# Performance work log

Measured on AMD Instinct MI355X. Metric: run time of the kernel, lower is better.

Reference implementation:

```python
import jax, jax.numpy as jnp
import numpy as np

B, L, E, H, K = 128, 512, 512, 256, 64


def setup_inputs() -> dict:
    key = jax.random.key(0)
    ks = jax.random.split(key, 13)
    s = 1.0 / np.sqrt(H)

    def u(k, shape):
        return jax.random.uniform(k, shape, jnp.float32, -s, s)

    return {
        "input_batch": jax.random.normal(ks[0], (B, L, E), jnp.float32),
        "labels": jax.random.randint(ks[1], (B, L), 0, K),
        "w_ih_f": u(ks[2], (4 * H, E)),
        "w_hh_f": u(ks[3], (4 * H, H)),
        "b_ih_f": u(ks[4], (4 * H,)),
        "b_hh_f": u(ks[5], (4 * H,)),
        "w_ih_b": u(ks[6], (4 * H, E)),
        "w_hh_b": u(ks[7], (4 * H, H)),
        "b_ih_b": u(ks[8], (4 * H,)),
        "b_hh_b": u(ks[9], (4 * H,)),
        "w_emit": u(ks[10], (K, 2 * H)),
        "b_emit": jnp.zeros((K,), jnp.float32),
        "transition": jax.random.normal(ks[11], (K, K), jnp.float32),
    }


def _lstm_dir(x, w_ih, w_hh, b_ih, b_hh):
    """One LSTM direction. x: (L,B,E) -> hidden states (L,B,H). PyTorch gate order i,f,g,o."""
    Hh = w_hh.shape[1]
    # input contribution for all timesteps at once: (L,B,4H)
    pre = jnp.einsum('lbe,ge->lbg', x, w_ih) + b_ih + b_hh

    def step(carry, p_t):
        h, c = carry
        g = p_t + h @ w_hh.T  # (B,4H)
        i, f, gg, o = jnp.split(g, 4, axis=-1)
        c = jax.nn.sigmoid(f) * c + jax.nn.sigmoid(i) * jnp.tanh(gg)
        h = jax.nn.sigmoid(o) * jnp.tanh(c)
        return (h, c), h

    init = (jnp.zeros((x.shape[1], Hh), x.dtype), jnp.zeros((x.shape[1], Hh), x.dtype))
    _, hs = jax.lax.scan(step, init, pre)
    return hs


def _bilstm_crf_loss(input_batch, labels, w_ih_f, w_hh_f, b_ih_f, b_hh_f,
                     w_ih_b, w_hh_b, b_ih_b, b_hh_b, w_emit, b_emit, transition):
    x = jnp.transpose(input_batch, (1, 0, 2))  # (L,B,E)
    h_f = _lstm_dir(x, w_ih_f, w_hh_f, b_ih_f, b_hh_f)
    h_b = _lstm_dir(x[::-1], w_ih_b, w_hh_b, b_ih_b, b_hh_b)[::-1]
    h = jnp.concatenate([h_f, h_b], axis=-1)  # (L,B,2H)
    emit = jnp.einsum('lbh,kh->b018'.replace('018', 'lk'), h, w_emit) + b_emit  # placeholder fixed below
    emit = jnp.einsum('lbh,kh->lbk', h, w_emit) + b_emit  # (L,B,K)
    emit = jnp.transpose(emit, (1, 0, 2))  # (B,L,K)

    # gold path score
    gold_emit = jnp.take_along_axis(emit, labels[:, :, None], axis=2)[:, :, 0]  # (B,L)
    gold_trans = transition[labels[:, :-1], labels[:, 1:]]  # (B,L-1)
    total_score = gold_emit.sum(axis=1) + gold_trans.sum(axis=1)  # (B,)

    # CRF forward algorithm (log partition), scan over timesteps 1..L-1
    def crf_step(d, e_t):
        # d: (B,K) log alpha; e_t: (B,K) emit at step t
        d = jax.nn.logsumexp(d[:, :, None] + transition[None, :, :] + e_t[:, None, :], axis=1)
        return d, None

    d0 = emit[:, 0]  # (B,K)
    dT, _ = jax.lax.scan(crf_step, d0, jnp.transpose(emit[:, 1:], (1, 0, 2)))
    log_z = jax.nn.logsumexp(dT, axis=1)  # (B,)
    return -(total_score - log_z)  # (B,)


def reference(input_batch, labels, w_ih_f, w_hh_f, b_ih_f, b_hh_f,
              w_ih_b, w_hh_b, b_ih_b, b_hh_b, w_emit, b_emit, transition):
    return _bilstm_crf_loss(input_batch, labels, w_ih_f, w_hh_f, b_ih_f, b_hh_f,
                            w_ih_b, w_hh_b, b_ih_b, b_hh_b, w_emit, b_emit, transition)
```

## Files before the change

kernel.cpp:

```cpp
#include <hip/hip_runtime.h>
#include <hip/hip_bf16.h>

#define B_   128
#define L_   512
#define E_   512
#define H_   256
#define K_   64
#define G4H  1024
#define LOG2E 1.4426950408889634f

typedef __bf16 bf16x8 __attribute__((ext_vector_type(8)));
typedef float  f32x4  __attribute__((ext_vector_type(4)));
typedef int    i32x8  __attribute__((ext_vector_type(8)));

__device__ inline unsigned short f2bf(float f) {
    unsigned int x = __builtin_bit_cast(unsigned int, f);
    unsigned int r = (x + 0x7fffu + ((x >> 16) & 1u)) >> 16;
    return (unsigned short)r;
}
__device__ inline float bf2f(unsigned short u) {
    unsigned int x = ((unsigned int)u) << 16;
    return __builtin_bit_cast(float, x);
}
__device__ inline unsigned int pack2(float lo, float hi) {
    return (unsigned int)f2bf(lo) | ((unsigned int)f2bf(hi) << 16);
}
__device__ inline float ex2(float x) { return __builtin_amdgcn_exp2f(x); }
__device__ inline float rcp_(float x) { return __builtin_amdgcn_rcpf(x); }

__device__ inline void gl_lds16(const unsigned short* g, unsigned short* l) {
    __builtin_amdgcn_global_load_lds(
        (const __attribute__((address_space(1))) unsigned int*)g,
        (__attribute__((address_space(3))) unsigned int*)l, 16, 0, 0);
}

__global__ void setup_convert(const float* __restrict__ whh_f, const float* __restrict__ whh_b,
                              const float* __restrict__ wemit,
                              const float* __restrict__ wihf, const float* __restrict__ wihb,
                              const float* __restrict__ bihf, const float* __restrict__ bhhf,
                              const float* __restrict__ bihb, const float* __restrict__ bhhb,
                              unsigned char* __restrict__ whh8,
                              unsigned short* __restrict__ wemit_bf,
                              unsigned short* __restrict__ wp,
                              float* __restrict__ bias_p) {
    int i = blockIdx.x * 256 + threadIdx.x;
    if (i < 262144) {
        int j = 2 * i;
        float v0 = (j < 262144) ? whh_f[j] : whh_b[j - 262144];
        float v1 = (j + 1 < 262144) ? whh_f[j + 1] : whh_b[j + 1 - 262144];
        int pk = __builtin_amdgcn_cvt_pk_fp8_f32(v0 * LOG2E, v1 * LOG2E, 0, false);
        ((unsigned short*)whh8)[i] = (unsigned short)(pk & 0xffff);
    }
    if (i < K_ * 2 * H_) wemit_bf[i] = f2bf(wemit[i]);
    if (i < 131072) {
        int rp = i >> 6;
        int k8 = (i & 63) * 8;
        int dd = rp >> 10, np = rp & 1023;
        int srow = (np & 3) * 256 + (np >> 2);
        const float* src = (dd == 0 ? wihf : wihb) + (size_t)srow * 512 + k8;
        float4 a  = *reinterpret_cast<const float4*>(src);
        float4 b2 = *reinterpret_cast<const float4*>(src + 4);
        uint4 pk = { pack2(a.x * LOG2E, a.y * LOG2E), pack2(a.z * LOG2E, a.w * LOG2E),
                     pack2(b2.x * LOG2E, b2.y * LOG2E), pack2(b2.z * LOG2E, b2.w * LOG2E) };
        *reinterpret_cast<uint4*>(wp + (size_t)rp * 512 + k8) = pk;
    }
    if (i < 2048) {
        int dd = i >> 10, np = i & 1023;
        int srow = (np & 3) * 256 + (np >> 2);
        bias_p[i] = ((dd == 0) ? (bihf[srow] + bhhf[srow]) : (bihb[srow] + bhhb[srow])) * LOG2E;
    }
}

__global__ void convert_x(const float* __restrict__ x, unsigned short* __restrict__ xb) {
    int i = blockIdx.x * 256 + threadIdx.x;
    float4 a = reinterpret_cast<const float4*>(x)[i * 2];
    float4 b = reinterpret_cast<const float4*>(x)[i * 2 + 1];
    uint4 p = { pack2(a.x, a.y), pack2(a.z, a.w), pack2(b.x, b.y), pack2(b.z, b.w) };
    reinterpret_cast<uint4*>(xb)[i] = p;
}

__global__ __launch_bounds__(256) void pre_gemm(
    const unsigned short* __restrict__ xb,
    const unsigned short* __restrict__ wp,
    const float* __restrict__ bias_p,
    unsigned short* __restrict__ pre3)
{
    __shared__ unsigned short A_lds[128 * 32];
    __shared__ unsigned short B_lds[128 * 32];

    int nt = blockIdx.x, mt = blockIdx.y;
    int tid = threadIdx.x;
    int n0 = nt * 128;
    int b  = mt >> 2, l0 = (mt & 3) * 128;
    int w = tid >> 6, lane = tid & 63;
    int q = lane >> 4, ln = lane & 15;
    int wm = (w >> 1) * 64, wn = (w & 1) * 64;

    f32x4 acc[4][4];
    #pragma unroll
    for (int i = 0; i < 4; ++i)
        #pragma unroll
        for (int j = 0; j < 4; ++j) acc[i][j] = (f32x4){0.f, 0.f, 0.f, 0.f};

    int r_ = tid >> 2, kp = (tid & 3) * 8;
    const unsigned short* asrc0 = xb + ((size_t)b * 512 + l0 + r_) * 512 + kp;
    const unsigned short* asrc1 = asrc0 + (size_t)64 * 512;
    const unsigned short* bsrc0 = wp + (size_t)(n0 + r_) * 512 + kp;
    const unsigned short* bsrc1 = bsrc0 + (size_t)64 * 512;
    unsigned short* adst0 = &A_lds[tid * 8];
    unsigned short* adst1 = &A_lds[2048 + tid * 8];
    unsigned short* bdst0 = &B_lds[tid * 8];
    unsigned short* bdst1 = &B_lds[2048 + tid * 8];

    for (int kc = 0; kc < 16; ++kc) {
        int k0 = kc * 32;
        gl_lds16(asrc0 + k0, adst0);
        gl_lds16(asrc1 + k0, adst1);
        gl_lds16(bsrc0 + k0, bdst0);
        gl_lds16(bsrc1 + k0, bdst1);
        __syncthreads();

        bf16x8 af[4], bfv[4];
        #pragma unroll
        for (int ms = 0; ms < 4; ++ms)
            af[ms] = *reinterpret_cast<const bf16x8*>(&A_lds[(wm + ms * 16 + ln) * 32 + q * 8]);
        #pragma unroll
        for (int ns = 0; ns < 4; ++ns)
            bfv[ns] = *reinterpret_cast<const bf16x8*>(&B_lds[(wn + ns * 16 + ln) * 32 + q * 8]);
        #pragma unroll
        for (int ms = 0; ms < 4; ++ms)
            #pragma unroll
            for (int ns = 0; ns < 4; ++ns)
                acc[ms][ns] = __builtin_amdgcn_mfma_f32_16x16x32_bf16(af[ms], bfv[ns], acc[ms][ns], 0, 0, 0);
        __syncthreads();
    }

    #pragma unroll
    for (int ns = 0; ns < 4; ++ns) {
        int n = n0 + wn + ns * 16 + ln;
        float bias = bias_p[n];
        int dsel = n >> 10, np = n & 1023;
        #pragma unroll
        for (int ms = 0; ms < 4; ++ms) {
            #pragma unroll
            for (int rg = 0; rg < 4; ++rg) {
                int l = l0 + wm + ms * 16 + q * 4 + rg;
                pre3[(((size_t)dsel * 128 + b) * 512 + l) * 1024 + np] = f2bf(acc[ms][ns][rg] + bias);
            }
        }
    }
}

__global__ __launch_bounds__(512, 2) void lstm_scan(
    const unsigned short* __restrict__ pre3,
    const unsigned char* __restrict__ whh8,
    unsigned short* __restrict__ hcat)
{
    __shared__ unsigned char h_lds[2][16 * 272];

    int wg = blockIdx.x;
    int d = wg >> 7, b = wg & 127;
    int tid = threadIdx.x, w = tid >> 6, lane = tid & 63;
    int q = lane >> 4, ln = lane & 15;

    const unsigned char* whh_d = whh8 + (size_t)d * (1024 * 256);
    const unsigned short* pre_wg = pre3 + ((size_t)d * 128 + b) * (512 * 1024);

    i32x8 wh[4][2][2];
    #pragma unroll
    for (int g = 0; g < 4; ++g)
        #pragma unroll
        for (int s = 0; s < 2; ++s) {
            int row = g * 256 + (w + 8 * s) * 16 + ln;
            #pragma unroll
            for (int kc = 0; kc < 2; ++kc)
                wh[g][s][kc] = *reinterpret_cast<const i32x8*>(
                    whh_d + (size_t)row * 256 + kc * 128 + q * 32);
        }

    for (int i = tid; i < (2 * 16 * 272) / 4; i += 512) ((int*)h_lds)[i] = 0;

    bool act = (lane < 32);
    int s_  = (lane >> 4) & 1;
    int col = (w + 8 * s_) * 16 + ln;

    ushort4 p0 = {0,0,0,0}, p1 = {0,0,0,0};
    if (act) {
        int la  = (d == 0) ? 0 : (L_ - 1);
        int lb_ = (d == 0) ? 1 : (L_ - 2);
        p0 = *reinterpret_cast<const ushort4*>(pre_wg + (size_t)la * 1024 + col * 4);
        p1 = *reinterpret_cast<const ushort4*>(pre_wg + (size_t)lb_ * 1024 + col * 4);
    }
    __syncthreads();

    float cst = 0.f;

    for (int t = 0; t < L_; ++t) {
        int p = t & 1;
        int l = (d == 0) ? t : (L_ - 1 - t);

        ushort4 p2 = {0,0,0,0};
        if (act) {
            int t2 = (t + 2 < L_) ? (t + 2) : (L_ - 1);
            int l2 = (d == 0) ? t2 : (L_ - 1 - t2);
            p2 = *reinterpret_cast<const ushort4*>(pre_wg + (size_t)l2 * 1024 + col * 4);
        }

        f32x4 acc[4][2];
        #pragma unroll
        for (int g = 0; g < 4; ++g) {
            acc[g][0] = (f32x4){0.f, 0.f, 0.f, 0.f};
            acc[g][1] = (f32x4){0.f, 0.f, 0.f, 0.f};
        }
        #pragma unroll
        for (int kc = 0; kc < 2; ++kc) {
            const unsigned char* ab = &h_lds[p][ln * 272 + kc * 128 + q * 32];
            uint4 a0 = *reinterpret_cast<const uint4*>(ab);
            uint4 a1 = *reinterpret_cast<const uint4*>(ab + 16);
            i32x8 af = { (int)a0.x, (int)a0.y, (int)a0.z, (int)a0.w,
                         (int)a1.x, (int)a1.y, (int)a1.z, (int)a1.w };
            #pragma unroll
            for (int g = 0; g < 4; ++g)
                #pragma unroll
                for (int s = 0; s < 2; ++s)
                    acc[g][s] = __builtin_amdgcn_mfma_scale_f32_16x16x128_f8f6f4(
                        af, wh[g][s][kc], acc[g][s], 0, 0,
                        0, 0x7f7f7f7f, 0, 0x7f7f7f7f);
        }

        float gv[4];
        #pragma unroll
        for (int g = 0; g < 4; ++g) {
            float lo = __shfl(acc[g][0][0], ln);
            float hi = __shfl(acc[g][1][0], ln);
            gv[g] = s_ ? hi : lo;
        }

        if (act) {
            float vi = gv[0] + bf2f(p0.x);
            float vf = gv[1] + bf2f(p0.y);
            float vg = gv[2] + bf2f(p0.z);
            float vo = gv[3] + bf2f(p0.w);
            float ei  = ex2(vi);
            float e2g = ex2(vg + vg);
            float itg = (ei * (e2g - 1.f)) * rcp_((1.f + ei) * (1.f + e2g));
            float sf  = rcp_(1.f + ex2(-vf));
            float cn  = fmaf(sf, cst, itg);
            cst = cn;
            float tc  = fmaf(-2.f, rcp_(1.f + ex2((2.f * LOG2E) * cn)), 1.f);
            float so  = rcp_(1.f + ex2(-vo));
            float hn  = so * tc;
            int pk = __builtin_amdgcn_cvt_pk_fp8_f32(hn, hn, 0, false);
            h_lds[p ^ 1][col] = (unsigned char)(pk & 0xff);
            hcat[((size_t)l * 128 + b) * 512 + d * 256 + col] = f2bf(hn);
        }
        __syncthreads();

        p0 = p1; p1 = p2;
    }
}

__global__ __launch_bounds__(256) void emit_gemm(
    const unsigned short* __restrict__ hcat,
    const unsigned short* __restrict__ wemit,
    const float* __restrict__ bemit,
    float* __restrict__ emit)
{
    int m0 = blockIdx.x * 64;
    int tid = threadIdx.x, w = tid >> 6, lane = tid & 63;
    int quad = lane >> 4, ln = lane & 15;
    int mrow = m0 + w * 16;

    f32x4 acc[4];
    #pragma unroll
    for (int i = 0; i < 4; ++i) acc[i] = (f32x4){0.f, 0.f, 0.f, 0.f};

    const unsigned short* arow = hcat + (size_t)(mrow + ln) * 512;
    #pragma unroll 4
    for (int kc = 0; kc < 16; ++kc) {
        bf16x8 af = *reinterpret_cast<const bf16x8*>(arow + kc * 32 + quad * 8);
        #pragma unroll
        for (int T = 0; T < 4; ++T) {
            bf16x8 bfv = *reinterpret_cast<const bf16x8*>(wemit + (size_t)(T * 16 + ln) * 512 + kc * 32 + quad * 8);
            acc[T] = __builtin_amdgcn_mfma_f32_16x16x32_bf16(af, bfv, acc[T], 0, 0, 0);
        }
    }
    #pragma unroll
    for (int T = 0; T < 4; ++T) {
        int k = T * 16 + ln;
        float bias = bemit[k];
        #pragma unroll
        for (int rg = 0; rg < 4; ++rg) {
            int m = mrow + quad * 4 + rg;
            int ll = m >> 7, bidx = m & 127;
            emit[((size_t)bidx * L_ + ll) * K_ + k] = acc[T][rg] + bias;
        }
    }
}

__global__ __launch_bounds__(64) void crf_kernel(
    const float* __restrict__ emit,
    const int* __restrict__ labels,
    const float* __restrict__ trans,
    float* __restrict__ out)
{
    __shared__ float els[64];
    int b = blockIdx.x, lane = threadIdx.x;
    const float* eb = emit + (size_t)b * L_ * K_;
    const int* lb = labels + (size_t)b * L_;

    float gold = 0.f;
    for (int t = lane; t < L_; t += 64) gold += eb[(size_t)t * K_ + lb[t]];
    for (int t = lane; t < L_ - 1; t += 64) gold += trans[lb[t] * K_ + lb[t + 1]];
    #pragma unroll
    for (int off = 32; off; off >>= 1) gold += __shfl_down(gold, off);

    float expT[64];
    #pragma unroll
    for (int i = 0; i < 64; ++i) expT[i] = __expf(trans[i * K_ + lane]);

    float dstate = eb[lane];
    float enext = eb[K_ + lane];
    for (int t = 1; t < L_; ++t) {
        float ecur = enext;
        if (t + 1 < L_) enext = eb[(size_t)(t + 1) * K_ + lane];
        float M = __builtin_amdgcn_readfirstlane(dstate);
        float e = __expf(dstate - M);
        __syncthreads();
        els[lane] = e;
        __syncthreads();
        float s = 0.f;
        #pragma unroll
        for (int i = 0; i < 64; i += 4) {
            float4 ev = *reinterpret_cast<const float4*>(&els[i]);
            s = fmaf(ev.x, expT[i], s);
            s = fmaf(ev.y, expT[i + 1], s);
            s = fmaf(ev.z, expT[i + 2], s);
            s = fmaf(ev.w, expT[i + 3], s);
        }
        dstate = M + __logf(s) + ecur;
    }
    float M = __builtin_amdgcn_readfirstlane(dstate);
    float e = __expf(dstate - M);
    float s = e;
    #pragma unroll
    for (int off = 32; off; off >>= 1) s += __shfl_xor(s, off);
    float logZ = M + __logf(s);
    if (lane == 0) out[b] = -(gold - logZ);
}

#define OFF_PRE    ((size_t)0)
#define OFF_EMIT   OFF_PRE
#define OFF_HCAT   ((size_t)268435456)
#define OFF_XB     OFF_HCAT
#define OFF_WHH8   ((size_t)(OFF_HCAT + 67108864))
#define OFF_WEMIT  ((size_t)(OFF_WHH8 + 524288))
#define OFF_WP     ((size_t)(OFF_WEMIT + 65536))
#define OFF_BIAS   ((size_t)(OFF_WP + 2097152))

extern "C" void kernel_launch(void* const* d_in, const int* in_sizes, int n_in,
                              void* d_out, int out_size, void* d_ws, size_t ws_size,
                              hipStream_t stream) {
    const float* x      = (const float*)d_in[0];
    const int*   labels = (const int*)d_in[1];
    const float* wihf   = (const float*)d_in[2];
    const float* whhf   = (const float*)d_in[3];
    const float* bihf   = (const float*)d_in[4];
    const float* bhhf   = (const float*)d_in[5];
    const float* wihb   = (const float*)d_in[6];
    const float* whhb   = (const float*)d_in[7];
    const float* bihb   = (const float*)d_in[8];
    const float* bhhb   = (const float*)d_in[9];
    const float* wemit  = (const float*)d_in[10];
    const float* bemit  = (const float*)d_in[11];
    const float* trans  = (const float*)d_in[12];
    float* out = (float*)d_out;

    char* ws = (char*)d_ws;
    unsigned short* pre3   = (unsigned short*)(ws + OFF_PRE);
    unsigned short* hcat   = (unsigned short*)(ws + OFF_HCAT);
    unsigned short* xb     = (unsigned short*)(ws + OFF_XB);
    float*          emit   = (float*)(ws + OFF_EMIT);
    unsigned char*  whh8   = (unsigned char*)(ws + OFF_WHH8);
    unsigned short* we_bf  = (unsigned short*)(ws + OFF_WEMIT);
    unsigned short* wp     = (unsigned short*)(ws + OFF_WP);
    float*          bias_p = (float*)(ws + OFF_BIAS);

    setup_convert<<<1024, 256, 0, stream>>>(whhf, whhb, wemit, wihf, wihb,
                                            bihf, bhhf, bihb, bhhb,
                                            whh8, we_bf, wp, bias_p);
    convert_x<<<16384, 256, 0, stream>>>(x, xb);
    pre_gemm<<<dim3(16, 512), 256, 0, stream>>>(xb, wp, bias_p, pre3);
    lstm_scan<<<256, 512, 0, stream>>>(pre3, whh8, hcat);
    emit_gemm<<<1024, 256, 0, stream>>>(hcat, we_bf, bemit, emit);
    crf_kernel<<<128, 64, 0, stream>>>(emit, labels, trans, out);
}
```

Measured before the change: 1.087 ms.

## Batch 16 sequences per LSTM workgroup via MFMA columns; double-buffer CRF LDS

The LSTM scan now uses the 16 MFMA columns for 16 batch elements in one workgroup, so 16 workgroups run instead of 256. Previously each workgroup handled a single sequence and wasted 15 of 16 MFMA columns. Each lane now computes four gate cells per slice, writes packed fp8/bf16 outputs, and prefetches pre-activations two steps ahead with an unrolled pair of steps. The CRF kernel double-buffers its LDS exchange to drop one barrier per step and splits the dot product into four accumulators. The risk is that only 16 CUs carry the serial scan, which adds more per-step latency per workgroup.

```diff
diff --git a/kernel.cpp b/kernel.cpp
--- a/kernel.cpp
+++ b/kernel.cpp
@@ -12,6 +12,7 @@
 typedef __bf16 bf16x8 __attribute__((ext_vector_type(8)));
 typedef float  f32x4  __attribute__((ext_vector_type(4)));
 typedef int    i32x8  __attribute__((ext_vector_type(8)));
+typedef unsigned short u16x8 __attribute__((ext_vector_type(8)));
 
 __device__ inline unsigned short f2bf(float f) {
     unsigned int x = __builtin_bit_cast(unsigned int, f);
@@ -159,12 +160,11 @@
     __shared__ unsigned char h_lds[2][16 * 272];
 
     int wg = blockIdx.x;
-    int d = wg >> 7, b = wg & 127;
+    int d = wg >> 3, b0 = (wg & 7) * 16;
     int tid = threadIdx.x, w = tid >> 6, lane = tid & 63;
     int q = lane >> 4, ln = lane & 15;
 
     const unsigned char* whh_d = whh8 + (size_t)d * (1024 * 256);
-    const unsigned short* pre_wg = pre3 + ((size_t)d * 128 + b) * (512 * 1024);
 
     i32x8 wh[4][2][2];
     #pragma unroll
@@ -180,30 +180,44 @@
 
     for (int i = tid; i < (2 * 16 * 272) / 4; i += 512) ((int*)h_lds)[i] = 0;
 
-    bool act = (lane < 32);
-    int s_  = (lane >> 4) & 1;
-    int col = (w + 8 * s_) * 16 + ln;
-
-    ushort4 p0 = {0,0,0,0}, p1 = {0,0,0,0};
-    if (act) {
-        int la  = (d == 0) ? 0 : (L_ - 1);
-        int lb_ = (d == 0) ? 1 : (L_ - 2);
-        p0 = *reinterpret_cast<const ushort4*>(pre_wg + (size_t)la * 1024 + col * 4);
-        p1 = *reinterpret_cast<const ushort4*>(pre_wg + (size_t)lb_ * 1024 + col * 4);
+    const unsigned short* pre_b = pre3 + (size_t)(d * 128 + b0 + ln) * (512 * 1024);
+    int nof[2] = { (w * 16 + q * 4) * 4, ((w + 8) * 16 + q * 4) * 4 };
+
+    u16x8 PA[2][2], PB[2][2];
+    {
+        int la  = d ? (L_ - 1) : 0;
+        int lb_ = d ? (L_ - 2) : 1;
+        #pragma unroll
+        for (int s = 0; s < 2; ++s) {
+            PA[s][0] = *reinterpret_cast<const u16x8*>(pre_b + (size_t)la  * 1024 + nof[s]);
+            PA[s][1] = *reinterpret_cast<const u16x8*>(pre_b + (size_t)la  * 1024 + nof[s] + 8);
+            PB[s][0] = *reinterpret_cast<const u16x8*>(pre_b + (size_t)lb_ * 1024 + nof[s]);
+            PB[s][1] = *reinterpret_cast<const u16x8*>(pre_b + (size_t)lb_ * 1024 + nof[s] + 8);
+        }
     }
     __syncthreads();
 
-    float cst = 0.f;
-
-    for (int t = 0; t < L_; ++t) {
+    float cst[2][4];
+    #pragma unroll
+    for (int s = 0; s < 2; ++s)
+        #pragma unroll
+        for (int rg = 0; rg < 4; ++rg) cst[s][rg] = 0.f;
+
+    auto step_fn = [&](int t, u16x8 (&P)[2][2], int t2) {
         int p = t & 1;
-        int l = (d == 0) ? t : (L_ - 1 - t);
-
-        ushort4 p2 = {0,0,0,0};
-        if (act) {
-            int t2 = (t + 2 < L_) ? (t + 2) : (L_ - 1);
-            int l2 = (d == 0) ? t2 : (L_ - 1 - t2);
-            p2 = *reinterpret_cast<const ushort4*>(pre_wg + (size_t)l2 * 1024 + col * 4);
+        int l = d ? (L_ - 1 - t) : t;
+
+        i32x8 af0, af1;
+        {
+            const unsigned char* ab = &h_lds[p][ln * 272 + q * 32];
+            uint4 a0 = *reinterpret_cast<const uint4*>(ab);
+            uint4 a1 = *reinterpret_cast<const uint4*>(ab + 16);
+            af0 = (i32x8){ (int)a0.x, (int)a0.y, (int)a0.z, (int)a0.w,
+                           (int)a1.x, (int)a1.y, (int)a1.z, (int)a1.w };
+            uint4 b0v = *reinterpret_cast<const uint4*>(ab + 128);
+            uint4 b1v = *reinterpret_cast<const uint4*>(ab + 144);
+            af1 = (i32x8){ (int)b0v.x, (int)b0v.y, (int)b0v.z, (int)b0v.w,
+                           (int)b1v.x, (int)b1v.y, (int)b1v.z, (int)b1v.w };
         }
 
         f32x4 acc[4][2];
@@ -213,50 +227,56 @@
             acc[g][1] = (f32x4){0.f, 0.f, 0.f, 0.f};
         }
         #pragma unroll
-        for (int kc = 0; kc < 2; ++kc) {
-            const unsigned char* ab = &h_lds[p][ln * 272 + kc * 128 + q * 32];
-            uint4 a0 = *reinterpret_cast<const uint4*>(ab);
-            uint4 a1 = *reinterpret_cast<const uint4*>(ab + 16);
-            i32x8 af = { (int)a0.x, (int)a0.y, (int)a0.z, (int)a0.w,
-                         (int)a1.x, (int)a1.y, (int)a1.z, (int)a1.w };
+        for (int g = 0; g < 4; ++g)
             #pragma unroll
-            for (int g = 0; g < 4; ++g)
-                #pragma unroll
-                for (int s = 0; s < 2; ++s)
-                    acc[g][s] = __builtin_amdgcn_mfma_scale_f32_16x16x128_f8f6f4(
-                        af, wh[g][s][kc], acc[g][s], 0, 0,
-                        0, 0x7f7f7f7f, 0, 0x7f7f7f7f);
-        }
-
-        float gv[4];
-        #pragma unroll
-        for (int g = 0; g < 4; ++g) {
-            float lo = __shfl(acc[g][0][0], ln);
-            float hi = __shfl(acc[g][1][0], ln);
-            gv[g] = s_ ? hi : lo;
-        }
-
-        if (act) {
-            float vi = gv[0] + bf2f(p0.x);
-            float vf = gv[1] + bf2f(p0.y);
-            float vg = gv[2] + bf2f(p0.z);
-            float vo = gv[3] + bf2f(p0.w);
-            float ei  = ex2(vi);
-            float e2g = ex2(vg + vg);
-            float itg = (ei * (e2g - 1.f)) * rcp_((1.f + ei) * (1.f + e2g));
-            float sf  = rcp_(1.f + ex2(-vf));
-            float cn  = fmaf(sf, cst, itg);
-            cst = cn;
-            float tc  = fmaf(-2.f, rcp_(1.f + ex2((2.f * LOG2E) * cn)), 1.f);
-            float so  = rcp_(1.f + ex2(-vo));
-            float hn  = so * tc;
-            int pk = __builtin_amdgcn_cvt_pk_fp8_f32(hn, hn, 0, false);
-            h_lds[p ^ 1][col] = (unsigned char)(pk & 0xff);
-            hcat[((size_t)l * 128 + b) * 512 + d * 256 + col] = f2bf(hn);
+            for (int s = 0; s < 2; ++s) {
+                acc[g][s] = __builtin_amdgcn_mfma_scale_f32_16x16x128_f8f6f4(
+                    wh[g][s][0], af0, acc[g][s], 0, 0, 0, 0x7f7f7f7f, 0, 0x7f7f7f7f);
+                acc[g][s] = __builtin_amdgcn_mfma_scale_f32_16x16x128_f8f6f4(
+                    wh[g][s][1], af1, acc[g][s], 0, 0, 0, 0x7f7f7f7f, 0, 0x7f7f7f7f);
+            }
+
+        #pragma unroll
+        for (int s = 0; s < 2; ++s) {
+            float hv[4];
+            #pragma unroll
+            for (int rg = 0; rg < 4; ++rg) {
+                float vi = acc[0][s][rg] + bf2f((unsigned short)P[s][rg >> 1][(rg & 1) * 4 + 0]);
+                float vf = acc[1][s][rg] + bf2f((unsigned short)P[s][rg >> 1][(rg & 1) * 4 + 1]);
+                float vg = acc[2][s][rg] + bf2f((unsigned short)P[s][rg >> 1][(rg & 1) * 4 + 2]);
+                float vo = acc[3][s][rg] + bf2f((unsigned short)P[s][rg >> 1][(rg & 1) * 4 + 3]);
+                float ei  = ex2(vi);
+                float e2g = ex2(vg + vg);
+                float itg = (ei * (e2g - 1.f)) * rcp_((1.f + ei) * (1.f + e2g));
+                float sf  = rcp_(1.f + ex2(-vf));
+                float cn  = fmaf(sf, cst[s][rg], itg);
+                cst[s][rg] = cn;
+                float tc  = fmaf(-2.f, rcp_(1.f + ex2((2.f * LOG2E) * cn)), 1.f);
+                float so  = rcp_(1.f + ex2(-vo));
+                hv[rg] = so * tc;
+            }
+            int colb = (w + 8 * s) * 16 + q * 4;
+            unsigned int w0 = (unsigned int)__builtin_amdgcn_cvt_pk_fp8_f32(hv[0], hv[1], 0, false);
+            unsigned int w1 = (unsigned int)__builtin_amdgcn_cvt_pk_fp8_f32(hv[2], hv[3], (int)w0, true);
+            *reinterpret_cast<unsigned int*>(&h_lds[p ^ 1][ln * 272 + colb]) = w1;
+            ushort4 hc = { f2bf(hv[0]), f2bf(hv[1]), f2bf(hv[2]), f2bf(hv[3]) };
+            *reinterpret_cast<ushort4*>(
+                hcat + ((size_t)l * 128 + b0 + ln) * 512 + d * 256 + colb) = hc;
+        }
+
+        int t2c = (t2 < L_ - 1) ? t2 : (L_ - 1);
+        int l2 = d ? (L_ - 1 - t2c) : t2c;
+        #pragma unroll
+        for (int s = 0; s < 2; ++s) {
+            P[s][0] = *reinterpret_cast<const u16x8*>(pre_b + (size_t)l2 * 1024 + nof[s]);
+            P[s][1] = *reinterpret_cast<const u16x8*>(pre_b + (size_t)l2 * 1024 + nof[s] + 8);
         }
         __syncthreads();
-
-        p0 = p1; p1 = p2;
+    };
+
+    for (int tt = 0; tt < L_; tt += 2) {
+        step_fn(tt,     PA, tt + 2);
+        step_fn(tt + 1, PB, tt + 3);
     }
 }
 
@@ -304,7 +324,7 @@
     const float* __restrict__ trans,
     float* __restrict__ out)
 {
-    __shared__ float els[64];
+    __shared__ float els[2][64];
     int b = blockIdx.x, lane = threadIdx.x;
     const float* eb = emit + (size_t)b * L_ * K_;
     const int* lb = labels + (size_t)b * L_;
@@ -326,19 +346,26 @@
         if (t + 1 < L_) enext = eb[(size_t)(t + 1) * K_ + lane];
         float M = __builtin_amdgcn_readfirstlane(dstate);
         float e = __expf(dstate - M);
+        float* el = els[t & 1];
+        el[lane] = e;
         __syncthreads();
-        els[lane] = e;
-        __syncthreads();
-        float s = 0.f;
-        #pragma unroll
-        for (int i = 0; i < 64; i += 4) {
-            float4 ev = *reinterpret_cast<const float4*>(&els[i]);
-            s = fmaf(ev.x, expT[i], s);
-            s = fmaf(ev.y, expT[i + 1], s);
-            s = fmaf(ev.z, expT[i + 2], s);
-            s = fmaf(ev.w, expT[i + 3], s);
-        }
-        dstate = M + __logf(s) + ecur;
+        float s0 = 0.f, s1 = 0.f, s2 = 0.f, s3 = 0.f;
+        #pragma unroll
+        for (int i = 0; i < 64; i += 16) {
+            float4 a0 = *reinterpret_cast<const float4*>(&el[i]);
+            float4 a1 = *reinterpret_cast<const float4*>(&el[i + 4]);
+            float4 a2 = *reinterpret_cast<const float4*>(&el[i + 8]);
+            float4 a3 = *reinterpret_cast<const float4*>(&el[i + 12]);
+            s0 = fmaf(a0.x, expT[i], s0);      s0 = fmaf(a0.y, expT[i + 1], s0);
+            s0 = fmaf(a0.z, expT[i + 2], s0);  s0 = fmaf(a0.w, expT[i + 3], s0);
+            s1 = fmaf(a1.x, expT[i + 4], s1);  s1 = fmaf(a1.y, expT[i + 5], s1);
+            s1 = fmaf(a1.z, expT[i + 6], s1);  s1 = fmaf(a1.w, expT[i + 7], s1);
+            s2 = fmaf(a2.x, expT[i + 8], s2);  s2 = fmaf(a2.y, expT[i + 9], s2);
+            s2 = fmaf(a2.z, expT[i + 10], s2); s2 = fmaf(a2.w, expT[i + 11], s2);
+            s3 = fmaf(a3.x, expT[i + 12], s3); s3 = fmaf(a3.y, expT[i + 13], s3);
+            s3 = fmaf(a3.z, expT[i + 14], s3); s3 = fmaf(a3.w, expT[i + 15], s3);
+        }
+        dstate = M + __logf((s0 + s1) + (s2 + s3)) + ecur;
     }
     float M = __builtin_amdgcn_readfirstlane(dstate);
     float e = __expf(dstate - M);
@@ -391,7 +418,7 @@
                                             whh8, we_bf, wp, bias_p);
     convert_x<<<16384, 256, 0, stream>>>(x, xb);
     pre_gemm<<<dim3(16, 512), 256, 0, stream>>>(xb, wp, bias_p, pre3);
-    lstm_scan<<<256, 512, 0, stream>>>(pre3, whh8, hcat);
+    lstm_scan<<<16, 512, 0, stream>>>(pre3, whh8, hcat);
     emit_gemm<<<1024, 256, 0, stream>>>(hcat, we_bf, bemit, emit);
     crf_kernel<<<128, 64, 0, stream>>>(emit, labels, trans, out);
 }
```

After: 1.889 ms. 1.74x slower.
